# Optimization experiments

Measured on AMD Instinct MI355X. Metric: run time of the kernel, lower is better.

Reference implementation:

```python
import jax, jax.numpy as jnp
import numpy as np

BN_EPS = 1e-5
K = 9  # 3x3 kernel points


def _conv3x3(x, w, b):
    out = jax.lax.conv_general_dilated(
        x, w, window_strides=(1, 1), padding=((1, 1), (1, 1)),
        dimension_numbers=('NCHW', 'OIHW', 'NCHW'))
    return out + b[None, :, None, None]


def _modulated_deform_conv(x, dy, dx, mask, w, b):
    # x: (B,C,H,W); dy,dx,mask: (B,K,H,W); w: (O,C,3,3); b: (O,)
    B, C, H, W = x.shape
    O = w.shape[0]
    ky = (jnp.arange(K) // 3 - 1).astype(x.dtype)  # kernel row offset per k
    kx = (jnp.arange(K) % 3 - 1).astype(x.dtype)   # kernel col offset per k
    gy = jnp.arange(H, dtype=x.dtype)[None, None, :, None]
    gx = jnp.arange(W, dtype=x.dtype)[None, None, None, :]
    py = gy + ky[None, :, None, None] + dy  # (B,K,H,W) sampling rows
    px = gx + kx[None, :, None, None] + dx  # (B,K,H,W) sampling cols
    y0 = jnp.floor(py)
    x0 = jnp.floor(px)
    ly = py - y0  # fractional parts
    lx = px - x0

    xf = x.reshape(B, C, H * W)

    def gather(yi, xi):
        # zero-padded gather of x at integer coords yi, xi (B,K,H,W)
        valid = (yi >= 0) & (yi <= H - 1) & (xi >= 0) & (xi <= W - 1)
        yc = jnp.clip(yi, 0, H - 1).astype(jnp.int32)
        xc = jnp.clip(xi, 0, W - 1).astype(jnp.int32)
        idx = (yc * W + xc).reshape(B, 1, K * H * W)
        g = jnp.take_along_axis(xf, idx, axis=2).reshape(B, C, K, H, W)
        return g * valid.astype(x.dtype).reshape(B, 1, K, H, W)

    w00 = ((1 - ly) * (1 - lx))[:, None]
    w01 = ((1 - ly) * lx)[:, None]
    w10 = (ly * (1 - lx))[:, None]
    w11 = (ly * lx)[:, None]
    # bilinear sample, modulated: (B,C,K,H,W)
    val = (gather(y0, x0) * w00 + gather(y0, x0 + 1) * w01
           + gather(y0 + 1, x0) * w10 + gather(y0 + 1, x0 + 1) * w11)
    val = val * mask[:, None]
    out = jnp.einsum('bckhw,ock->bohw', val, w.reshape(O, C, K))
    return out + b[None, :, None, None]


def _forward(input_x, w_off, b_off, w, b, gamma, beta, rmean, rvar):
    off = _conv3x3(input_x, w_off, b_off)        # (B, 27, H, W)
    offset = off[:, :2 * K]
    dy = offset[:, 0::2]                          # (B, 9, H, W)
    dx = offset[:, 1::2]
    mask = jax.nn.sigmoid(off[:, 2 * K:])         # (B, 9, H, W)
    y = _modulated_deform_conv(input_x, dy, dx, mask, w, b)
    # BatchNorm (eval mode, running stats) + ReLU
    scale = gamma / jnp.sqrt(rvar + BN_EPS)
    y = y * scale[None, :, None, None] + (beta - rmean * scale)[None, :, None, None]
    return jax.nn.relu(y)


def setup_inputs() -> dict:
    key = jax.random.key(0)
    ks = jax.random.split(key, 4)
    B, CHI, CHO, H, W = 4, 256, 256, 96, 96
    input_x = jax.random.normal(ks[0], (B, CHI, H, W), dtype=jnp.float32)
    w_off = jax.random.normal(ks[1], (3 * K, CHI, 3, 3), dtype=jnp.float32) * 0.01
    b_off = jnp.zeros((3 * K,), dtype=jnp.float32)
    w = jax.random.normal(ks[2], (CHO, CHI, 3, 3), dtype=jnp.float32) * 0.02
    b = jnp.zeros((CHO,), dtype=jnp.float32)
    gamma = jnp.ones((CHO,), dtype=jnp.float32)
    beta = jnp.zeros((CHO,), dtype=jnp.float32)
    rmean = jnp.zeros((CHO,), dtype=jnp.float32)
    rvar = jnp.ones((CHO,), dtype=jnp.float32)
    return {'input_x': input_x, 'w_off': w_off, 'b_off': b_off, 'w': w, 'b': b,
            'gamma': gamma, 'beta': beta, 'rmean': rmean, 'rvar': rvar}


def reference(input_x, w_off, b_off, w, b, gamma, beta, rmean, rvar):
    return _forward(input_x, w_off, b_off, w, b, gamma, beta, rmean, rvar)
```

## Files before the change

### kernel.cpp

```cpp
#include <hip/hip_runtime.h>
#include <cmath>

#define HH 96
#define WW 96
#define HWsz 9216
#define CCH 256
#define OO 256
#define MTOT 36864
#define NTAP 9

using short8 = __attribute__((ext_vector_type(8))) short;
using f32x4  = __attribute__((ext_vector_type(4))) float;

__device__ __forceinline__ unsigned short f2bf(float f) {
    unsigned u = __float_as_uint(f);
    u += 0x7fff + ((u >> 16) & 1);
    return (unsigned short)(u >> 16);
}

__global__ __launch_bounds__(256) void prep_kernel(
    const float* __restrict__ w, const float* __restrict__ w_off,
    const float* __restrict__ gamma, const float* __restrict__ beta,
    const float* __restrict__ rmean, const float* __restrict__ rvar,
    const float* __restrict__ bconv,
    unsigned short* __restrict__ wq, unsigned short* __restrict__ wqA,
    float* __restrict__ sc2, float* __restrict__ sh2)
{
    int gid = blockIdx.x * 256 + threadIdx.x;
    if (gid < 589824) {
        int j = gid & 7, o = (gid >> 3) & 255, kh = (gid >> 11) & 3;
        int cc = (gid >> 13) & 7, t = gid >> 16;
        int c = cc * 32 + kh * 8 + j;
        wq[gid] = f2bf(w[(o * 256 + c) * 9 + t]);
        return;
    }
    gid -= 589824;
    if (gid < 73728) {
        int j = gid & 7, o = (gid >> 3) & 31, kh = (gid >> 8) & 3;
        int cc = (gid >> 10) & 7, t = gid >> 13;
        int c = cc * 32 + kh * 8 + j;
        wqA[gid] = (o < 27) ? f2bf(w_off[(o * 256 + c) * 9 + t]) : (unsigned short)0;
        return;
    }
    gid -= 73728;
    if (gid < 256) {
        float s = gamma[gid] * rsqrtf(rvar[gid] + 1e-5f);
        sc2[gid] = s;
        sh2[gid] = beta[gid] - rmean[gid] * s + bconv[gid] * s;
    }
}

__global__ __launch_bounds__(256) void build_table(
    const float* __restrict__ off, int4* __restrict__ tbi, float4* __restrict__ tbw)
{
    int e = blockIdx.x * 256 + threadIdx.x;
    if (e >= MTOT * NTAP) return;
    int p = e / 9, t = e - p * 9;
    int b = p / HWsz, hw = p - b * HWsz;
    int h = hw / WW, x = hw % WW;
    const float* ob = off + ((size_t)b * 32) * HWsz + hw;
    float dy = ob[(2 * t) * HWsz];
    float dx = ob[(2 * t + 1) * HWsz];
    float ml = ob[(18 + t) * HWsz];
    float m = 1.f / (1.f + __expf(-ml));
    float py = (float)(h + t / 3 - 1) + dy;
    float px = (float)(x + t % 3 - 1) + dx;
    float y0f = floorf(py), x0f = floorf(px);
    float ly = py - y0f, lx = px - x0f;
    int y0 = (int)y0f, x0 = (int)x0f;
    int y1 = y0 + 1, x1 = x0 + 1;
    bool vy0 = (y0 >= 0) && (y0 <= HH - 1), vy1 = (y1 >= 0) && (y1 <= HH - 1);
    bool vx0 = (x0 >= 0) && (x0 <= WW - 1), vx1 = (x1 >= 0) && (x1 <= WW - 1);
    int yc0 = min(max(y0, 0), HH - 1), yc1 = min(max(y1, 0), HH - 1);
    int xc0 = min(max(x0, 0), WW - 1), xc1 = min(max(x1, 0), WW - 1);
    float w00 = (1.f - ly) * (1.f - lx) * m;
    float w01 = (1.f - ly) * lx * m;
    float w10 = ly * (1.f - lx) * m;
    float w11 = ly * lx * m;
    int4 iv; iv.x = yc0 * WW + xc0; iv.y = yc0 * WW + xc1; iv.z = yc1 * WW + xc0; iv.w = yc1 * WW + xc1;
    float4 wv;
    wv.x = (vy0 && vx0) ? w00 : 0.f;
    wv.y = (vy0 && vx1) ? w01 : 0.f;
    wv.z = (vy1 && vx0) ? w10 : 0.f;
    wv.w = (vy1 && vx1) ? w11 : 0.f;
    tbi[(size_t)t * MTOT + p] = iv;
    tbw[(size_t)t * MTOT + p] = wv;
}

template<int NOCH, int NCOR, int WM, int WN, bool PASS2>
__global__ __launch_bounds__(256, 2) void gemm_dcn(
    const float* __restrict__ x,
    const unsigned short* __restrict__ wq,
    const int4* __restrict__ tbi, const float4* __restrict__ tbw,
    const float* __restrict__ ep0, const float* __restrict__ ep1,
    float* __restrict__ outp)
{
    constexpr int NWM = 4 / WM;
    __shared__ __align__(16) unsigned short Alds[2][64][40];

    const int tid  = threadIdx.x;
    const int wid  = tid >> 6;
    const int lane = tid & 63;
    const int l15  = lane & 15;
    const int kh   = lane >> 4;
    const int mslab = wid % NWM;
    const int nslab = wid / NWM;

    const int bid  = blockIdx.x;
    const int mblk = (bid & 7) * ((int)gridDim.x >> 3) + (bid >> 3);
    const int p0   = mblk * 64;

    const int pg   = p0 + lane;
    const int img  = p0 / HWsz;
    const int hw0  = pg - img * HWsz;
    const int ph   = hw0 / WW;
    const int pxx  = hw0 - ph * WW;
    const float* __restrict__ xim = x + (size_t)img * CCH * HWsz;

    f32x4 acc[WM][WN];
    #pragma unroll
    for (int m = 0; m < WM; ++m)
        #pragma unroll
        for (int n = 0; n < WN; ++n)
            acc[m][n] = f32x4{0.f, 0.f, 0.f, 0.f};

    int ti0 = 0, ti1 = 0, ti2 = 0, ti3 = 0;
    float tw0 = 0.f, tw1 = 0.f, tw2 = 0.f, tw3 = 0.f;
    float xv0[8], xv1[8], xv2[8], xv3[8];
    short8 bcur[WN], bnxt[WN];

    auto LOADTAB = [&](int t) {
        if constexpr (NCOR == 4) {
            int4 iv = tbi[(size_t)t * MTOT + pg];
            float4 wv = tbw[(size_t)t * MTOT + pg];
            ti0 = iv.x; ti1 = iv.y; ti2 = iv.z; ti3 = iv.w;
            tw0 = wv.x; tw1 = wv.y; tw2 = wv.z; tw3 = wv.w;
        } else {
            int yy = ph + t / 3 - 1, xx = pxx + t % 3 - 1;
            bool v = (yy >= 0) && (yy < HH) && (xx >= 0) && (xx < WW);
            ti0 = v ? yy * WW + xx : 0;
            tw0 = v ? 1.f : 0.f;
        }
    };

    auto PRELOAD = [&](int t, int cc) {
        const unsigned cb = (unsigned)(cc * 32 + wid * 8) * HWsz;
        #pragma unroll
        for (int i = 0; i < 8; ++i) {
            unsigned o = cb + (unsigned)i * HWsz;
            xv0[i] = xim[o + ti0];
            if constexpr (NCOR == 4) {
                xv1[i] = xim[o + ti1];
                xv2[i] = xim[o + ti2];
                xv3[i] = xim[o + ti3];
            }
        }
        #pragma unroll
        for (int n = 0; n < WN; ++n) {
            int och = nslab * WN * 16 + n * 16 + l15;
            bnxt[n] = *(const short8*)(wq + (size_t)(((t * 8 + cc) * 4 + kh) * NOCH + och) * 8);
        }
    };

    auto PACK = [&](int buf) {
        short8 pk;
        #pragma unroll
        for (int i = 0; i < 8; ++i) {
            float v = tw0 * xv0[i];
            if constexpr (NCOR == 4)
                v += tw1 * xv1[i] + tw2 * xv2[i] + tw3 * xv3[i];
            pk[i] = (short)f2bf(v);
        }
        *(short8*)&Alds[buf][lane][wid * 8] = pk;
    };

    LOADTAB(0);
    PRELOAD(0, 0);
    int buf = 0;
    for (int it = 0; it < NTAP * 8; ++it) {
        #pragma unroll
        for (int n = 0; n < WN; ++n) bcur[n] = bnxt[n];
        PACK(buf);
        int nit = it + 1;
        if (nit < NTAP * 8) {
            int nt = nit >> 3, ncc = nit & 7;
            if (ncc == 0) LOADTAB(nt);
            PRELOAD(nt, ncc);
        }
        asm volatile("s_waitcnt lgkmcnt(0)" ::: "memory");
        __builtin_amdgcn_s_barrier();
        __builtin_amdgcn_sched_barrier(0);
        short8 af[WM];
        #pragma unroll
        for (int m = 0; m < WM; ++m)
            af[m] = *(const short8*)&Alds[buf][mslab * WM * 16 + m * 16 + l15][kh * 8];
        #pragma unroll
        for (int m = 0; m < WM; ++m)
            #pragma unroll
            for (int n = 0; n < WN; ++n)
                acc[m][n] = __builtin_amdgcn_mfma_f32_16x16x32_bf16(af[m], bcur[n], acc[m][n], 0, 0, 0);
        buf ^= 1;
    }

    const int ohwb = p0 - img * HWsz;
    #pragma unroll
    for (int n = 0; n < WN; ++n) {
        int och = nslab * WN * 16 + n * 16 + l15;
        float s0 = 0.f, s1 = 0.f;
        if constexpr (PASS2) { s0 = ep0[och]; s1 = ep1[och]; }
        else { s1 = (och < 27) ? ep0[och] : 0.f; }
        #pragma unroll
        for (int m = 0; m < WM; ++m) {
            int ohw = ohwb + mslab * WM * 16 + m * 16 + kh * 4;
            float4 vv;
            if constexpr (PASS2) {
                vv.x = fmaxf(fmaf(acc[m][n][0], s0, s1), 0.f);
                vv.y = fmaxf(fmaf(acc[m][n][1], s0, s1), 0.f);
                vv.z = fmaxf(fmaf(acc[m][n][2], s0, s1), 0.f);
                vv.w = fmaxf(fmaf(acc[m][n][3], s0, s1), 0.f);
                *(float4*)&outp[((size_t)img * OO + och) * HWsz + ohw] = vv;
            } else {
                if (och < 27) {
                    vv.x = acc[m][n][0] + s1;
                    vv.y = acc[m][n][1] + s1;
                    vv.z = acc[m][n][2] + s1;
                    vv.w = acc[m][n][3] + s1;
                    *(float4*)&outp[((size_t)img * 32 + och) * HWsz + ohw] = vv;
                }
            }
        }
    }
}

extern "C" void kernel_launch(void* const* d_in, const int* in_sizes, int n_in,
                              void* d_out, int out_size, void* d_ws, size_t ws_size,
                              hipStream_t stream) {
    const float* input_x = (const float*)d_in[0];
    const float* w_off   = (const float*)d_in[1];
    const float* b_off   = (const float*)d_in[2];
    const float* w       = (const float*)d_in[3];
    const float* b       = (const float*)d_in[4];
    const float* gamma   = (const float*)d_in[5];
    const float* beta    = (const float*)d_in[6];
    const float* rmean   = (const float*)d_in[7];
    const float* rvar    = (const float*)d_in[8];
    float* out = (float*)d_out;

    char* p = (char*)d_ws;
    auto alloc = [&](size_t bytes) {
        char* r = p;
        p += (bytes + 255) & ~(size_t)255;
        return r;
    };
    unsigned short* wq  = (unsigned short*)alloc(589824 * 2);
    unsigned short* wqA = (unsigned short*)alloc(73728 * 2);
    int4*   tdi = (int4*)alloc((size_t)331776 * 16);
    float4* tdw = (float4*)alloc((size_t)331776 * 16);
    float* offb = (float*)alloc((size_t)4 * 32 * 9216 * 4);
    float* sc2 = (float*)alloc(256 * 4);
    float* sh2 = (float*)alloc(256 * 4);

    prep_kernel<<<2593, 256, 0, stream>>>(w, w_off, gamma, beta, rmean, rvar, b,
                                          wq, wqA, sc2, sh2);
    gemm_dcn<32, 1, 1, 2, false><<<576, 256, 0, stream>>>(input_x, wqA, nullptr, nullptr, b_off, nullptr, offb);
    build_table<<<1296, 256, 0, stream>>>(offb, tdi, tdw);
    gemm_dcn<256, 4, 4, 4, true><<<576, 256, 0, stream>>>(input_x, wq, tdi, tdw, sc2, sh2, out);
}
```

Measured before the change: 500.2 us.

## Drop LDS staging; each wave gathers its own 16-pixel A fragment directly

The GEMM kernel no longer stages bilinear-sampled activations through double-buffered LDS with block barriers. Each wave now owns 16 pixels across all 256 output channels and builds its MFMA A fragment in registers, reading weight fragments straight from global memory with no software pipelining. The table is compacted to two row-base indices with adjacent-column loads (x clamped to W-2, column weights adjusted), and launch bounds are raised to 3 blocks per CU. This removes LDS traffic and barrier stalls, but each wave now reloads the full weight matrix (a larger B-operand read volume) and no longer prefetches gathers ahead of the MFMAs.

Result: slower. 649.8 us (+29.9%).

```diff
diff --git a/kernel.cpp b/kernel.cpp
--- a/kernel.cpp
+++ b/kernel.cpp
@@ -51,7 +51,7 @@
 }
 
 __global__ __launch_bounds__(256) void build_table(
-    const float* __restrict__ off, int4* __restrict__ tbi, float4* __restrict__ tbw)
+    const float* __restrict__ off, int2* __restrict__ tbi, float4* __restrict__ tbw)
 {
     int e = blockIdx.x * 256 + threadIdx.x;
     if (e >= MTOT * NTAP) return;
@@ -68,165 +68,114 @@
     float y0f = floorf(py), x0f = floorf(px);
     float ly = py - y0f, lx = px - x0f;
     int y0 = (int)y0f, x0 = (int)x0f;
-    int y1 = y0 + 1, x1 = x0 + 1;
-    bool vy0 = (y0 >= 0) && (y0 <= HH - 1), vy1 = (y1 >= 0) && (y1 <= HH - 1);
-    bool vx0 = (x0 >= 0) && (x0 <= WW - 1), vx1 = (x1 >= 0) && (x1 <= WW - 1);
-    int yc0 = min(max(y0, 0), HH - 1), yc1 = min(max(y1, 0), HH - 1);
-    int xc0 = min(max(x0, 0), WW - 1), xc1 = min(max(x1, 0), WW - 1);
-    float w00 = (1.f - ly) * (1.f - lx) * m;
-    float w01 = (1.f - ly) * lx * m;
-    float w10 = ly * (1.f - lx) * m;
-    float w11 = ly * lx * m;
-    int4 iv; iv.x = yc0 * WW + xc0; iv.y = yc0 * WW + xc1; iv.z = yc1 * WW + xc0; iv.w = yc1 * WW + xc1;
+    int y1 = y0 + 1;
+    int xb = min(max(x0, 0), WW - 2);
+    float cw0 = (xb == x0) ? (1.f - lx) : ((xb == x0 + 1) ? lx : 0.f);
+    float cw1 = (xb + 1 == x0) ? (1.f - lx) : ((xb + 1 == x0 + 1) ? lx : 0.f);
+    float rt = (y0 >= 0 && y0 <= HH - 1) ? (1.f - ly) : 0.f;
+    float rb = (y1 >= 0 && y1 <= HH - 1) ? ly : 0.f;
+    int yt = min(max(y0, 0), HH - 1), yb = min(max(y1, 0), HH - 1);
+    int2 iv; iv.x = yt * WW + xb; iv.y = yb * WW + xb;
     float4 wv;
-    wv.x = (vy0 && vx0) ? w00 : 0.f;
-    wv.y = (vy0 && vx1) ? w01 : 0.f;
-    wv.z = (vy1 && vx0) ? w10 : 0.f;
-    wv.w = (vy1 && vx1) ? w11 : 0.f;
+    wv.x = rt * cw0 * m; wv.y = rt * cw1 * m;
+    wv.z = rb * cw0 * m; wv.w = rb * cw1 * m;
     tbi[(size_t)t * MTOT + p] = iv;
     tbw[(size_t)t * MTOT + p] = wv;
 }
 
-template<int NOCH, int NCOR, int WM, int WN, bool PASS2>
-__global__ __launch_bounds__(256, 2) void gemm_dcn(
+template<int NOCH, int NCOR, bool PASS2>
+__global__ __launch_bounds__(256, 3) void gemm_dcn(
     const float* __restrict__ x,
     const unsigned short* __restrict__ wq,
-    const int4* __restrict__ tbi, const float4* __restrict__ tbw,
+    const int2* __restrict__ tbi, const float4* __restrict__ tbw,
     const float* __restrict__ ep0, const float* __restrict__ ep1,
     float* __restrict__ outp)
 {
-    constexpr int NWM = 4 / WM;
-    __shared__ __align__(16) unsigned short Alds[2][64][40];
-
+    constexpr int NMF = NOCH / 16;
     const int tid  = threadIdx.x;
     const int wid  = tid >> 6;
     const int lane = tid & 63;
     const int l15  = lane & 15;
     const int kh   = lane >> 4;
-    const int mslab = wid % NWM;
-    const int nslab = wid / NWM;
 
     const int bid  = blockIdx.x;
     const int mblk = (bid & 7) * ((int)gridDim.x >> 3) + (bid >> 3);
     const int p0   = mblk * 64;
-
-    const int pg   = p0 + lane;
+    const int wp0  = p0 + wid * 16;
+    const int pg   = wp0 + l15;
     const int img  = p0 / HWsz;
     const int hw0  = pg - img * HWsz;
     const int ph   = hw0 / WW;
     const int pxx  = hw0 - ph * WW;
     const float* __restrict__ xim = x + (size_t)img * CCH * HWsz;
 
-    f32x4 acc[WM][WN];
+    f32x4 acc[NMF];
     #pragma unroll
-    for (int m = 0; m < WM; ++m)
-        #pragma unroll
-        for (int n = 0; n < WN; ++n)
-            acc[m][n] = f32x4{0.f, 0.f, 0.f, 0.f};
-
-    int ti0 = 0, ti1 = 0, ti2 = 0, ti3 = 0;
-    float tw0 = 0.f, tw1 = 0.f, tw2 = 0.f, tw3 = 0.f;
-    float xv0[8], xv1[8], xv2[8], xv3[8];
-    short8 bcur[WN], bnxt[WN];
-
-    auto LOADTAB = [&](int t) {
+    for (int n = 0; n < NMF; ++n) acc[n] = f32x4{0.f, 0.f, 0.f, 0.f};
+
+    for (int t = 0; t < NTAP; ++t) {
+        int it_ = 0, ib_ = 0;
+        float w00_ = 0.f, w01_ = 0.f, w10_ = 0.f, w11_ = 0.f;
         if constexpr (NCOR == 4) {
-            int4 iv = tbi[(size_t)t * MTOT + pg];
+            int2 iv = tbi[(size_t)t * MTOT + pg];
             float4 wv = tbw[(size_t)t * MTOT + pg];
-            ti0 = iv.x; ti1 = iv.y; ti2 = iv.z; ti3 = iv.w;
-            tw0 = wv.x; tw1 = wv.y; tw2 = wv.z; tw3 = wv.w;
+            it_ = iv.x; ib_ = iv.y;
+            w00_ = wv.x; w01_ = wv.y; w10_ = wv.z; w11_ = wv.w;
         } else {
             int yy = ph + t / 3 - 1, xx = pxx + t % 3 - 1;
             bool v = (yy >= 0) && (yy < HH) && (xx >= 0) && (xx < WW);
-            ti0 = v ? yy * WW + xx : 0;
-            tw0 = v ? 1.f : 0.f;
+            it_ = v ? yy * WW + xx : 0;
+            w00_ = v ? 1.f : 0.f;
         }
-    };
-
-    auto PRELOAD = [&](int t, int cc) {
-        const unsigned cb = (unsigned)(cc * 32 + wid * 8) * HWsz;
-        #pragma unroll
-        for (int i = 0; i < 8; ++i) {
-            unsigned o = cb + (unsigned)i * HWsz;
-            xv0[i] = xim[o + ti0];
+        #pragma unroll 1
+        for (int cc = 0; cc < 8; ++cc) {
+            const unsigned cb = (unsigned)(cc * 32 + kh * 8) * HWsz;
+            float va[8];
             if constexpr (NCOR == 4) {
-                xv1[i] = xim[o + ti1];
-                xv2[i] = xim[o + ti2];
-                xv3[i] = xim[o + ti3];
+                #pragma unroll
+                for (int j = 0; j < 8; ++j) {
+                    const float* pt = xim + cb + (unsigned)j * HWsz;
+                    float t0 = pt[it_], t1 = pt[it_ + 1];
+                    float b0 = pt[ib_], b1 = pt[ib_ + 1];
+                    va[j] = w00_ * t0 + w01_ * t1 + w10_ * b0 + w11_ * b1;
+                }
+            } else {
+                #pragma unroll
+                for (int j = 0; j < 8; ++j)
+                    va[j] = w00_ * xim[cb + (unsigned)j * HWsz + it_];
+            }
+            short8 af;
+            #pragma unroll
+            for (int j = 0; j < 8; ++j) af[j] = (short)f2bf(va[j]);
+            const unsigned short* wb = wq + (size_t)(((t * 8 + cc) * 4 + kh) * NOCH) * 8;
+            #pragma unroll
+            for (int n = 0; n < NMF; ++n) {
+                short8 bfr = *(const short8*)(wb + (n * 16 + l15) * 8);
+                acc[n] = __builtin_amdgcn_mfma_f32_16x16x32_bf16(af, bfr, acc[n], 0, 0, 0);
             }
         }
-        #pragma unroll
-        for (int n = 0; n < WN; ++n) {
-            int och = nslab * WN * 16 + n * 16 + l15;
-            bnxt[n] = *(const short8*)(wq + (size_t)(((t * 8 + cc) * 4 + kh) * NOCH + och) * 8);
-        }
-    };
-
-    auto PACK = [&](int buf) {
-        short8 pk;
-        #pragma unroll
-        for (int i = 0; i < 8; ++i) {
-            float v = tw0 * xv0[i];
-            if constexpr (NCOR == 4)
-                v += tw1 * xv1[i] + tw2 * xv2[i] + tw3 * xv3[i];
-            pk[i] = (short)f2bf(v);
-        }
-        *(short8*)&Alds[buf][lane][wid * 8] = pk;
-    };
-
-    LOADTAB(0);
-    PRELOAD(0, 0);
-    int buf = 0;
-    for (int it = 0; it < NTAP * 8; ++it) {
-        #pragma unroll
-        for (int n = 0; n < WN; ++n) bcur[n] = bnxt[n];
-        PACK(buf);
-        int nit = it + 1;
-        if (nit < NTAP * 8) {
-            int nt = nit >> 3, ncc = nit & 7;
-            if (ncc == 0) LOADTAB(nt);
-            PRELOAD(nt, ncc);
-        }
-        asm volatile("s_waitcnt lgkmcnt(0)" ::: "memory");
-        __builtin_amdgcn_s_barrier();
-        __builtin_amdgcn_sched_barrier(0);
-        short8 af[WM];
-        #pragma unroll
-        for (int m = 0; m < WM; ++m)
-            af[m] = *(const short8*)&Alds[buf][mslab * WM * 16 + m * 16 + l15][kh * 8];
-        #pragma unroll
-        for (int m = 0; m < WM; ++m)
-            #pragma unroll
-            for (int n = 0; n < WN; ++n)
-                acc[m][n] = __builtin_amdgcn_mfma_f32_16x16x32_bf16(af[m], bcur[n], acc[m][n], 0, 0, 0);
-        buf ^= 1;
-    }
-
-    const int ohwb = p0 - img * HWsz;
+    }
+
+    const int opix = wp0 - img * HWsz + kh * 4;
     #pragma unroll
-    for (int n = 0; n < WN; ++n) {
-        int och = nslab * WN * 16 + n * 16 + l15;
-        float s0 = 0.f, s1 = 0.f;
-        if constexpr (PASS2) { s0 = ep0[och]; s1 = ep1[och]; }
-        else { s1 = (och < 27) ? ep0[och] : 0.f; }
-        #pragma unroll
-        for (int m = 0; m < WM; ++m) {
-            int ohw = ohwb + mslab * WM * 16 + m * 16 + kh * 4;
-            float4 vv;
-            if constexpr (PASS2) {
-                vv.x = fmaxf(fmaf(acc[m][n][0], s0, s1), 0.f);
-                vv.y = fmaxf(fmaf(acc[m][n][1], s0, s1), 0.f);
-                vv.z = fmaxf(fmaf(acc[m][n][2], s0, s1), 0.f);
-                vv.w = fmaxf(fmaf(acc[m][n][3], s0, s1), 0.f);
-                *(float4*)&outp[((size_t)img * OO + och) * HWsz + ohw] = vv;
-            } else {
-                if (och < 27) {
-                    vv.x = acc[m][n][0] + s1;
-                    vv.y = acc[m][n][1] + s1;
-                    vv.z = acc[m][n][2] + s1;
-                    vv.w = acc[m][n][3] + s1;
-                    *(float4*)&outp[((size_t)img * 32 + och) * HWsz + ohw] = vv;
-                }
+    for (int n = 0; n < NMF; ++n) {
+        int och = n * 16 + l15;
+        float4 vv;
+        if constexpr (PASS2) {
+            float s0 = ep0[och], s1 = ep1[och];
+            vv.x = fmaxf(fmaf(acc[n][0], s0, s1), 0.f);
+            vv.y = fmaxf(fmaf(acc[n][1], s0, s1), 0.f);
+            vv.z = fmaxf(fmaf(acc[n][2], s0, s1), 0.f);
+            vv.w = fmaxf(fmaf(acc[n][3], s0, s1), 0.f);
+            *(float4*)&outp[((size_t)img * OO + och) * HWsz + opix] = vv;
+        } else {
+            if (och < 27) {
+                float s1 = ep0[och];
+                vv.x = acc[n][0] + s1;
+                vv.y = acc[n][1] + s1;
+                vv.z = acc[n][2] + s1;
+                vv.w = acc[n][3] + s1;
+                *(float4*)&outp[((size_t)img * 32 + och) * HWsz + opix] = vv;
             }
         }
     }
@@ -254,7 +203,7 @@
     };
     unsigned short* wq  = (unsigned short*)alloc(589824 * 2);
     unsigned short* wqA = (unsigned short*)alloc(73728 * 2);
-    int4*   tdi = (int4*)alloc((size_t)331776 * 16);
+    int2*   tdi = (int2*)alloc((size_t)331776 * 8);
     float4* tdw = (float4*)alloc((size_t)331776 * 16);
     float* offb = (float*)alloc((size_t)4 * 32 * 9216 * 4);
     float* sc2 = (float*)alloc(256 * 4);
@@ -262,7 +211,7 @@
 
     prep_kernel<<<2593, 256, 0, stream>>>(w, w_off, gamma, beta, rmean, rvar, b,
                                           wq, wqA, sc2, sh2);
-    gemm_dcn<32, 1, 1, 2, false><<<576, 256, 0, stream>>>(input_x, wqA, nullptr, nullptr, b_off, nullptr, offb);
+    gemm_dcn<32, 1, false><<<576, 256, 0, stream>>>(input_x, wqA, nullptr, nullptr, b_off, nullptr, offb);
     build_table<<<1296, 256, 0, stream>>>(offb, tdi, tdw);
-    gemm_dcn<256, 4, 4, 4, true><<<576, 256, 0, stream>>>(input_x, wq, tdi, tdw, sc2, sh2, out);
-}
+    gemm_dcn<256, 4, true><<<576, 256, 0, stream>>>(input_x, wq, tdi, tdw, sc2, sh2, out);
+}
```
